# Kernel tuning notes

Measured on AMD Instinct MI355X. Metric: run time of the kernel, lower is better.

## Reference

```python
import jax, jax.numpy as jnp
import numpy as np

H, W, C_IN, C_OUT, B = 256, 256, 64, 64, 2
NEG_SLOPE = 0.2


def make_grid_edges(h, w, b):
    """8-neighborhood grid edges + self-loops (GATConv add_self_loops), batched with node offsets."""
    idx = np.arange(h * w).reshape(h, w)
    src_l, dst_l = [], []
    for dr in (-1, 0, 1):
        for dc in (-1, 0, 1):
            rs = slice(max(0, -dr), h - max(0, dr))
            cs = slice(max(0, -dc), w - max(0, dc))
            dst = idx[rs, cs]
            src = idx[rs.start + dr:rs.stop + dr, cs.start + dc:cs.stop + dc]
            src_l.append(src.ravel())
            dst_l.append(dst.ravel())
    s = np.concatenate(src_l)
    d = np.concatenate(dst_l)
    offs = (np.arange(b) * h * w)[:, None]
    return (s[None] + offs).ravel().astype(np.int32), (d[None] + offs).ravel().astype(np.int32)


def setup_inputs() -> dict:
    key = jax.random.key(0)
    ks = jax.random.split(key, 7)
    x = jax.random.normal(ks[0], (B, C_IN, H, W), dtype=jnp.float32)
    pos_w = jax.random.normal(ks[1], (2, C_IN), dtype=jnp.float32) * (1.0 / np.sqrt(2.0))
    pos_b = jax.random.normal(ks[2], (C_IN,), dtype=jnp.float32) * 0.1
    lin_w = jax.random.normal(ks[3], (C_IN, C_OUT), dtype=jnp.float32) * (1.0 / np.sqrt(C_IN))
    att_src = jax.random.normal(ks[4], (C_OUT,), dtype=jnp.float32) * (1.0 / np.sqrt(C_OUT))
    att_dst = jax.random.normal(ks[5], (C_OUT,), dtype=jnp.float32) * (1.0 / np.sqrt(C_OUT))
    bias = jax.random.normal(ks[6], (C_OUT,), dtype=jnp.float32) * 0.1
    es, ed = make_grid_edges(H, W, B)
    return {"x": x, "pos_w": pos_w, "pos_b": pos_b, "lin_w": lin_w,
            "att_src": att_src, "att_dst": att_dst, "bias": bias,
            "edge_src": jnp.asarray(es), "edge_dst": jnp.asarray(ed)}


def reference(x, pos_w, pos_b, lin_w, att_src, att_dst, bias, edge_src, edge_dst):
    b, c, h, w = x.shape
    n = h * w
    num_nodes = b * n
    # positional encoding: pos[h,w] = (y, x) in [-1,1]
    px = jnp.linspace(-1.0, 1.0, w)
    py = jnp.linspace(-1.0, 1.0, h)
    gx, gy = jnp.meshgrid(px, py, indexing="xy")          # (H, W)
    pos = jnp.stack([gy, gx], axis=-1)                     # (H, W, 2)
    pe = pos @ pos_w + pos_b                               # (H, W, C)
    xg = (x + pe.transpose(2, 0, 1)[None]).transpose(0, 2, 3, 1).reshape(num_nodes, c)
    # GATConv, heads=1: linear transform, per-edge attention logits
    hfeat = xg @ lin_w                                     # (BN, Cout)
    a_src = hfeat @ att_src                                # (BN,)
    a_dst = hfeat @ att_dst                                # (BN,)
    e = jax.nn.leaky_relu(a_src[edge_src] + a_dst[edge_dst], NEG_SLOPE)  # (E,)
    # segment softmax over incoming edges of each target node
    m = jax.ops.segment_max(e, edge_dst, num_segments=num_nodes)
    p = jnp.exp(e - m[edge_dst])
    s = jax.ops.segment_sum(p, edge_dst, num_segments=num_nodes)
    alpha = p / s[edge_dst]                                # (E,)
    # scatter-add aggregation of weighted messages
    out = jax.ops.segment_sum(alpha[:, None] * hfeat[edge_src], edge_dst,
                              num_segments=num_nodes) + bias
    return out.reshape(b, h, w, -1).transpose(0, 3, 1, 2)
```

## Files before the change

kernel.cpp:

```cpp
#include <hip/hip_runtime.h>

#define HGT 256
#define WID 256
#define CH  64
#define NB  2
#define HW  (HGT * WID)
#define NODES (NB * HW)
#define NEG_SLOPE 0.2f

__global__ __launch_bounds__(256) void gat_feat(
    const float* __restrict__ x, const float* __restrict__ pos_w,
    const float* __restrict__ pos_b, const float* __restrict__ lin_w,
    const float* __restrict__ att_src, const float* __restrict__ att_dst,
    float* __restrict__ hfeat, float* __restrict__ asrc, float* __restrict__ adst)
{
    __shared__ float W0[CH], W1[CH], Bc[CH];
    __shared__ float red_s[4][64], red_d[4][64];

    const int tid = threadIdx.x;
    const int tx  = tid & 63;
    const int ty  = tid >> 6;

    const int bid   = blockIdx.x;
    const int chunk = bid & 3;
    const int bi    = bid >> 2;
    const int i     = bi & (HGT - 1);
    const int b     = bi >> 8;
    const int j     = chunk * 64 + tx;

    if (tid < CH) {
        float w0 = 0.f, w1 = 0.f, bc = 0.f;
        for (int ci = 0; ci < CH; ++ci) {
            float lwv = lin_w[ci * CH + tid];
            w0 = fmaf(pos_w[ci],      lwv, w0);
            w1 = fmaf(pos_w[CH + ci], lwv, w1);
            bc = fmaf(pos_b[ci],      lwv, bc);
        }
        W0[tid] = w0; W1[tid] = w1; Bc[tid] = bc;
    }
    __syncthreads();

    const int cob = __builtin_amdgcn_readfirstlane(ty) * 16;

    float acc[16];
    #pragma unroll
    for (int k = 0; k < 16; ++k) acc[k] = 0.f;

    const float* xb = x + (size_t)b * CH * HW + (size_t)i * WID + j;
    const float* lw = lin_w + cob;
    #pragma unroll 8
    for (int ci = 0; ci < CH; ++ci) {
        float xv = xb[(size_t)ci * HW];
        #pragma unroll
        for (int k = 0; k < 16; ++k)
            acc[k] = fmaf(xv, lw[ci * CH + k], acc[k]);
    }

    const float py = -1.f + (2.f / 255.f) * (float)i;
    const float px = -1.f + (2.f / 255.f) * (float)j;

    float as = 0.f, ad = 0.f;
    float* hb = hfeat + ((size_t)b * CH + cob) * HW + (size_t)i * WID + j;
    #pragma unroll
    for (int k = 0; k < 16; ++k) {
        const int co = cob + k;
        float h = acc[k] + py * W0[co] + px * W1[co] + Bc[co];
        hb[(size_t)k * HW] = h;
        as = fmaf(h, att_src[co], as);
        ad = fmaf(h, att_dst[co], ad);
    }

    red_s[ty][tx] = as; red_d[ty][tx] = ad;
    __syncthreads();
    if (ty == 0) {
        const size_t node = (size_t)bi * WID + j;
        asrc[node] = red_s[0][tx] + red_s[1][tx] + red_s[2][tx] + red_s[3][tx];
        adst[node] = red_d[0][tx] + red_d[1][tx] + red_d[2][tx] + red_d[3][tx];
    }
}

__global__ __launch_bounds__(256) void gat_aggr(
    const float* __restrict__ hfeat, const float* __restrict__ asrc,
    const float* __restrict__ adst, const float* __restrict__ bias,
    float* __restrict__ out)
{
    const int tid = threadIdx.x;
    const int tx  = tid & 63;
    const int ty  = tid >> 6;

    const int raw = blockIdx.x;
    const int wg  = (raw & 7) * 256 + (raw >> 3);

    const int chunk = wg & 3;
    const int bi    = wg >> 2;
    const int i     = bi & (HGT - 1);
    const int b     = bi >> 8;
    const int j     = chunk * 64 + tx;
    const int node  = bi * WID + j;

    const float adv = adst[node];

    float w[9];
    int   off[9];
    float m = -1e30f;
    #pragma unroll
    for (int t = 0; t < 9; ++t) {
        const int dr = t / 3 - 1, dc = t % 3 - 1;
        const int r = i + dr, c = j + dc;
        const bool ok = (r >= 0) && (r < HGT) && (c >= 0) && (c < WID);
        off[t] = ok ? (dr * WID + dc) : 0;
        float ev = -1e30f;
        if (ok) {
            ev = asrc[node + off[t]] + adv;
            ev = (ev >= 0.f) ? ev : NEG_SLOPE * ev;
        }
        w[t] = ev;
        m = fmaxf(m, ev);
    }

    float s = 0.f;
    #pragma unroll
    for (int t = 0; t < 9; ++t) {
        float p = (w[t] > -1e29f) ? __expf(w[t] - m) : 0.f;
        w[t] = p; s += p;
    }
    const float inv = 1.f / s;
    #pragma unroll
    for (int t = 0; t < 9; ++t) w[t] *= inv;

    const int cob = __builtin_amdgcn_readfirstlane(ty) * 16;
    const float* hb = hfeat + ((size_t)b * CH + cob) * HW + (size_t)i * WID + j;
    float*       ob = out   + ((size_t)b * CH + cob) * HW + (size_t)i * WID + j;

    float acc[16];
    #pragma unroll
    for (int k = 0; k < 16; ++k) acc[k] = 0.f;

    #pragma unroll
    for (int t = 0; t < 9; ++t) {
        const float* hp = hb + off[t];
        const float  a  = w[t];
        #pragma unroll
        for (int k = 0; k < 16; ++k)
            acc[k] = fmaf(a, hp[(size_t)k * HW], acc[k]);
    }

    #pragma unroll
    for (int k = 0; k < 16; ++k)
        ob[(size_t)k * HW] = acc[k] + bias[cob + k];
}

extern "C" void kernel_launch(void* const* d_in, const int* in_sizes, int n_in,
                              void* d_out, int out_size, void* d_ws, size_t ws_size,
                              hipStream_t stream) {
    const float* x       = (const float*)d_in[0];
    const float* pos_w   = (const float*)d_in[1];
    const float* pos_b   = (const float*)d_in[2];
    const float* lin_w   = (const float*)d_in[3];
    const float* att_src = (const float*)d_in[4];
    const float* att_dst = (const float*)d_in[5];
    const float* bias    = (const float*)d_in[6];

    float* out   = (float*)d_out;
    float* hfeat = (float*)d_ws;
    float* asrc  = hfeat + (size_t)NODES * CH;
    float* adst  = asrc + NODES;

    gat_feat<<<dim3(2048), dim3(256), 0, stream>>>(
        x, pos_w, pos_b, lin_w, att_src, att_dst, hfeat, asrc, adst);
    gat_aggr<<<dim3(2048), dim3(256), 0, stream>>>(
        hfeat, asrc, adst, bias, out);
}
```

Before: 137.1 us.

## Store hfeat as bf16 in channel-quad layout and re-split aggregation blocks

The intermediate feature map is packed to bf16 with round-to-nearest-even and stored as groups of four channels per node (uint2), halving the workspace write and the 9-neighbour gather traffic. The feature kernel stages x through LDS and swizzles block order. The aggregation kernel now has each wavefront handle four channels with 8192 blocks, and the softmax normalisation is folded into the weights. The cost is bf16 rounding error in the aggregated output and recomputation of attention weights per channel quad.

```diff
diff --git a/kernel.cpp b/kernel.cpp
--- a/kernel.cpp
+++ b/kernel.cpp
@@ -8,12 +8,21 @@
 #define NODES (NB * HW)
 #define NEG_SLOPE 0.2f
 
+
+__device__ __forceinline__ unsigned short f2bf(float f) {
+    union { float f; unsigned u; } v; v.f = f;
+    unsigned r = v.u + 0x7FFF + ((v.u >> 16) & 1);
+    return (unsigned short)(r >> 16);
+}
+
 __global__ __launch_bounds__(256) void gat_feat(
     const float* __restrict__ x, const float* __restrict__ pos_w,
     const float* __restrict__ pos_b, const float* __restrict__ lin_w,
     const float* __restrict__ att_src, const float* __restrict__ att_dst,
-    float* __restrict__ hfeat, float* __restrict__ asrc, float* __restrict__ adst)
+    unsigned short* __restrict__ hfeat, float* __restrict__ asrc,
+    float* __restrict__ adst)
 {
+    __shared__ float xs[CH][64];
     __shared__ float W0[CH], W1[CH], Bc[CH];
     __shared__ float red_s[4][64], red_d[4][64];
 
@@ -21,12 +30,21 @@
     const int tx  = tid & 63;
     const int ty  = tid >> 6;
 
-    const int bid   = blockIdx.x;
-    const int chunk = bid & 3;
-    const int bi    = bid >> 2;
+    const int raw = blockIdx.x;
+    const int wg  = (raw & 7) * 256 + (raw >> 3);
+    const int chunk = wg & 3;
+    const int bi    = wg >> 2;
     const int i     = bi & (HGT - 1);
     const int b     = bi >> 8;
     const int j     = chunk * 64 + tx;
+    const int hw    = i * WID + j;
+
+    const float* xb = x + (size_t)b * CH * HW + hw;
+    #pragma unroll
+    for (int r = 0; r < 16; ++r) {
+        const int ci = ty * 16 + r;
+        xs[ci][tx] = xb[(size_t)ci * HW];
+    }
 
     if (tid < CH) {
         float w0 = 0.f, w1 = 0.f, bc = 0.f;
@@ -46,41 +64,46 @@
     #pragma unroll
     for (int k = 0; k < 16; ++k) acc[k] = 0.f;
 
-    const float* xb = x + (size_t)b * CH * HW + (size_t)i * WID + j;
     const float* lw = lin_w + cob;
-    #pragma unroll 8
+    #pragma unroll
     for (int ci = 0; ci < CH; ++ci) {
-        float xv = xb[(size_t)ci * HW];
+        const float xv = xs[ci][tx];
         #pragma unroll
         for (int k = 0; k < 16; ++k)
             acc[k] = fmaf(xv, lw[ci * CH + k], acc[k]);
     }
 
-    const float py = -1.f + (2.f / 255.f) * (float)i;
-    const float px = -1.f + (2.f / 255.f) * (float)j;
+    const float py  = -1.f + (2.f / 255.f) * (float)i;
+    const float pxv = -1.f + (2.f / 255.f) * (float)j;
 
     float as = 0.f, ad = 0.f;
-    float* hb = hfeat + ((size_t)b * CH + cob) * HW + (size_t)i * WID + j;
+    unsigned pk[8];
     #pragma unroll
     for (int k = 0; k < 16; ++k) {
         const int co = cob + k;
-        float h = acc[k] + py * W0[co] + px * W1[co] + Bc[co];
-        hb[(size_t)k * HW] = h;
+        const float h = acc[k] + py * W0[co] + pxv * W1[co] + Bc[co];
         as = fmaf(h, att_src[co], as);
         ad = fmaf(h, att_dst[co], ad);
+        const unsigned short bf = f2bf(h);
+        if (k & 1) pk[k >> 1] |= (unsigned)bf << 16;
+        else       pk[k >> 1]  = bf;
     }
+    uint2* hq = (uint2*)hfeat + (size_t)(b * 16 + (cob >> 2)) * HW + hw;
+    #pragma unroll
+    for (int qq = 0; qq < 4; ++qq)
+        hq[(size_t)qq * HW] = make_uint2(pk[2 * qq], pk[2 * qq + 1]);
 
     red_s[ty][tx] = as; red_d[ty][tx] = ad;
     __syncthreads();
     if (ty == 0) {
-        const size_t node = (size_t)bi * WID + j;
+        const int node = b * HW + hw;
         asrc[node] = red_s[0][tx] + red_s[1][tx] + red_s[2][tx] + red_s[3][tx];
         adst[node] = red_d[0][tx] + red_d[1][tx] + red_d[2][tx] + red_d[3][tx];
     }
 }
 
 __global__ __launch_bounds__(256) void gat_aggr(
-    const float* __restrict__ hfeat, const float* __restrict__ asrc,
+    const unsigned short* __restrict__ hfeat, const float* __restrict__ asrc,
     const float* __restrict__ adst, const float* __restrict__ bias,
     float* __restrict__ out)
 {
@@ -89,14 +112,16 @@
     const int ty  = tid >> 6;
 
     const int raw = blockIdx.x;
-    const int wg  = (raw & 7) * 256 + (raw >> 3);
-
-    const int chunk = wg & 3;
-    const int bi    = wg >> 2;
+    const int wg  = (raw & 7) * 1024 + (raw >> 3);
+    const int qg    = wg & 3;
+    const int chunk = (wg >> 2) & 3;
+    const int bi    = wg >> 4;
     const int i     = bi & (HGT - 1);
     const int b     = bi >> 8;
     const int j     = chunk * 64 + tx;
-    const int node  = bi * WID + j;
+    const int hw    = i * WID + j;
+    const int node  = b * HW + hw;
+    const int q     = __builtin_amdgcn_readfirstlane(qg * 4 + ty);
 
     const float adv = adst[node];
 
@@ -121,33 +146,29 @@
     float s = 0.f;
     #pragma unroll
     for (int t = 0; t < 9; ++t) {
-        float p = (w[t] > -1e29f) ? __expf(w[t] - m) : 0.f;
+        const float p = (w[t] > -1e29f) ? __expf(w[t] - m) : 0.f;
         w[t] = p; s += p;
     }
     const float inv = 1.f / s;
-    #pragma unroll
-    for (int t = 0; t < 9; ++t) w[t] *= inv;
 
-    const int cob = __builtin_amdgcn_readfirstlane(ty) * 16;
-    const float* hb = hfeat + ((size_t)b * CH + cob) * HW + (size_t)i * WID + j;
-    float*       ob = out   + ((size_t)b * CH + cob) * HW + (size_t)i * WID + j;
+    const uint2* hq = (const uint2*)hfeat + (size_t)(b * 16 + q) * HW + hw;
 
-    float acc[16];
-    #pragma unroll
-    for (int k = 0; k < 16; ++k) acc[k] = 0.f;
-
+    float a0 = 0.f, a1 = 0.f, a2 = 0.f, a3 = 0.f;
     #pragma unroll
     for (int t = 0; t < 9; ++t) {
-        const float* hp = hb + off[t];
-        const float  a  = w[t];
-        #pragma unroll
-        for (int k = 0; k < 16; ++k)
-            acc[k] = fmaf(a, hp[(size_t)k * HW], acc[k]);
+        const uint2 v  = hq[off[t]];
+        const float wt = w[t] * inv;
+        a0 = fmaf(wt, __uint_as_float(v.x << 16),         a0);
+        a1 = fmaf(wt, __uint_as_float(v.x & 0xffff0000u), a1);
+        a2 = fmaf(wt, __uint_as_float(v.y << 16),         a2);
+        a3 = fmaf(wt, __uint_as_float(v.y & 0xffff0000u), a3);
     }
 
-    #pragma unroll
-    for (int k = 0; k < 16; ++k)
-        ob[(size_t)k * HW] = acc[k] + bias[cob + k];
+    float* ob = out + (size_t)(b * CH + q * 4) * HW + hw;
+    ob[0 * (size_t)HW] = a0 + bias[q * 4 + 0];
+    ob[1 * (size_t)HW] = a1 + bias[q * 4 + 1];
+    ob[2 * (size_t)HW] = a2 + bias[q * 4 + 2];
+    ob[3 * (size_t)HW] = a3 + bias[q * 4 + 3];
 }
 
 extern "C" void kernel_launch(void* const* d_in, const int* in_sizes, int n_in,
@@ -161,13 +182,13 @@
     const float* att_dst = (const float*)d_in[5];
     const float* bias    = (const float*)d_in[6];
 
-    float* out   = (float*)d_out;
-    float* hfeat = (float*)d_ws;
-    float* asrc  = hfeat + (size_t)NODES * CH;
-    float* adst  = asrc + NODES;
+    float* out = (float*)d_out;
+    unsigned short* hfeat = (unsigned short*)d_ws;
+    float* asrc = (float*)((char*)d_ws + (size_t)NODES * CH * 2);
+    float* adst = asrc + NODES;
 
     gat_feat<<<dim3(2048), dim3(256), 0, stream>>>(
         x, pos_w, pos_b, lin_w, att_src, att_dst, hfeat, asrc, adst);
-    gat_aggr<<<dim3(2048), dim3(256), 0, stream>>>(
+    gat_aggr<<<dim3(8192), dim3(256), 0, stream>>>(
         hfeat, asrc, adst, bias, out);
 }
```

New measurement: 150.2 us. 9.6% more time.
